# Optimization experiments

Hardware: AMD Instinct MI355X
Metric: run time of the kernel (lower is better)

## Reference

```python
import jax, jax.numpy as jnp
import numpy as np

B, T_IN, T_OUT, V, C = 2048, 10, 25, 22, 3
D = V * C            # embed / gru hidden = 66
H = 3                # attention heads
HD = D // H          # head dim = 22
EPS = 1e-5
DIMS = [(C, 64), (64, 32), (32, 64), (64, C)]


def _bn(x, g, b):
    # eval-mode BatchNorm2d with default running stats (mean=0, var=1)
    return x * (g / jnp.sqrt(1.0 + EPS))[None, :, None, None] + b[None, :, None, None]


def _gcn_layer(x, A, Tm, cw, cb, g, bt, rw, rb, rg, rbt, pre):
    # x: (N, Cin, T, V); STSGCN ST_GCNN_layer with 1x1 conv (kernel [1,1])
    res = _bn(jnp.einsum('nctv,oc->notv', x, rw) + rb[None, :, None, None], rg, rbt)
    y = jnp.einsum('nctv,vtq->ncqv', x, Tm)   # temporal mixing
    y = jnp.einsum('nctv,tvw->nctw', y, A)    # spatial (joint) mixing
    y = _bn(jnp.einsum('nctv,oc->notv', y, cw) + cb[None, :, None, None], g, bt)
    y = y + res
    return jnp.where(y >= 0, y, pre * y)      # PReLU (scalar slope)


def setup_inputs() -> dict:
    key = jax.random.key(0)
    ks = iter(jax.random.split(key, 64))
    def rn(shape, s=0.05):
        return jax.random.normal(next(ks), shape, dtype=jnp.float32) * s
    d = {"x": rn((B, T_IN, V, C), 1.0)}
    d["A"] = rn((4, T_IN, V, V), 0.2)
    d["Tm"] = rn((4, V, T_IN, T_IN), 0.3)
    d["pre"] = jnp.full((4,), 0.25, jnp.float32)
    for i, (ci, co) in enumerate(DIMS):
        d[f"cw{i}"] = rn((co, ci), 0.1)
        d[f"cb{i}"] = rn((co,), 0.1)
        d[f"g{i}"] = jnp.ones((co,), jnp.float32)
        d[f"bt{i}"] = jnp.zeros((co,), jnp.float32)
        d[f"rw{i}"] = rn((co, ci), 0.1)
        d[f"rb{i}"] = rn((co,), 0.1)
        d[f"rg{i}"] = jnp.ones((co,), jnp.float32)
        d[f"rbt{i}"] = jnp.zeros((co,), jnp.float32)
    d["gru_wi"] = rn((3 * D, D)); d["gru_wh"] = rn((3 * D, D))
    d["gru_bi"] = rn((3 * D,));   d["gru_bh"] = rn((3 * D,))
    d["qkv_w"] = rn((3 * D, D)); d["qkv_b"] = rn((3 * D,))
    d["ow"] = rn((D, D)); d["ob"] = rn((D,))
    d["lw"] = rn((D, 2 * D)); d["lb"] = rn((D,))
    return d


def _forward(x, A, Tm, pre, cws, cbs, gs, bts, rws, rbs, rgs, rbts,
             gru_wi, gru_wh, gru_bi, gru_bh, qkv_w, qkv_b, ow, ob, lw, lb):
    raw = x.reshape(B, T_IN, D)                 # (N,T,V*C), joint-major flatten
    h = jnp.transpose(x, (0, 3, 1, 2))          # (N,C,T,V)
    for i in range(4):
        h = _gcn_layer(h, A[i], Tm[i], cws[i], cbs[i], gs[i], bts[i],
                       rws[i], rbs[i], rgs[i], rbts[i], pre[i])
    enc = jnp.transpose(h, (0, 2, 3, 1)).reshape(B, T_IN, D)  # (N,T,V*C)

    wq, wk, wv = qkv_w[:D], qkv_w[D:2 * D], qkv_w[2 * D:]
    bq, bk, bv = qkv_b[:D], qkv_b[D:2 * D], qkv_b[2 * D:]
    # K,V of encoder sequence are constant across decode steps: project once
    k = (enc @ wk.T + bk).reshape(B, T_IN, H, HD)
    v = (enc @ wv.T + bv).reshape(B, T_IN, H, HD)
    scale = 1.0 / jnp.sqrt(jnp.float32(HD))

    def gru(inp, hprev):
        gi = inp @ gru_wi.T + gru_bi
        gh = hprev @ gru_wh.T + gru_bh
        ir, iz, inn = jnp.split(gi, 3, axis=-1)
        hr, hz, hn = jnp.split(gh, 3, axis=-1)
        r = jax.nn.sigmoid(ir + hr)
        z = jax.nn.sigmoid(iz + hz)
        n = jnp.tanh(inn + r * hn)
        return (1.0 - z) * n + z * hprev

    def step(carry, _):
        hs, tp = carry
        hs = gru(tp, hs)
        q = ((hs @ wq.T + bq) * scale).reshape(B, H, HD)
        scores = jnp.einsum('bhd,bthd->bht', q, k)
        attn = jax.nn.softmax(scores, axis=-1)
        ctx = jnp.einsum('bht,bthd->bhd', attn, v).reshape(B, D) @ ow.T + ob
        pred = jnp.concatenate([hs, ctx], axis=-1) @ lw.T + lb + tp  # residual
        return (hs, pred), pred

    h0 = enc[:, -1, :]
    tp0 = raw[:, -1, :]
    _, preds = jax.lax.scan(step, (h0, tp0), None, length=T_OUT)
    out = jnp.transpose(preds, (1, 0, 2))       # (N, T_out, D)
    return out.reshape(B, T_OUT, V, C)


def reference(x, A, Tm, pre,
              cw0, cb0, g0, bt0, rw0, rb0, rg0, rbt0,
              cw1, cb1, g1, bt1, rw1, rb1, rg1, rbt1,
              cw2, cb2, g2, bt2, rw2, rb2, rg2, rbt2,
              cw3, cb3, g3, bt3, rw3, rb3, rg3, rbt3,
              gru_wi, gru_wh, gru_bi, gru_bh, qkv_w, qkv_b, ow, ob, lw, lb):
    return _forward(x, A, Tm, pre,
                    [cw0, cw1, cw2, cw3], [cb0, cb1, cb2, cb3],
                    [g0, g1, g2, g3], [bt0, bt1, bt2, bt3],
                    [rw0, rw1, rw2, rw3], [rb0, rb1, rb2, rb3],
                    [rg0, rg1, rg2, rg3], [rbt0, rbt1, rbt2, rbt3],
                    gru_wi, gru_wh, gru_bi, gru_bh, qkv_w, qkv_b, ow, ob, lw, lb)
```

## Files before the change

kernel.cpp:

```cpp
#include <hip/hip_runtime.h>

#define DEV static __device__ __forceinline__


struct EncW {
  const float* cw[4]; const float* cb[4]; const float* g[4]; const float* bt[4];
  const float* rw[4]; const float* rb[4]; const float* rg[4]; const float* rbt[4];
};


template<int CI, int CO, int OGRAN>
DEV void gcn_orig(int tid,
    const float* __restrict__ cw, const float* __restrict__ cb,
    const float* __restrict__ gg, const float* __restrict__ bt,
    const float* __restrict__ rw, const float* __restrict__ rb,
    const float* __restrict__ rg, const float* __restrict__ rbt,
    const float* __restrict__ TmL, const float* __restrict__ AL, float preL,
    float* __restrict__ act, float* __restrict__ S,
    float* __restrict__ rmul, float* __restrict__ radd,
    float* __restrict__ cmul, float* __restrict__ cadd)
{
  constexpr int COP8 = (CO + 7) & ~7;
  constexpr int NT = (CO / OGRAN) * 55;
  constexpr int RWN = CI * COP8;
  static_assert(RWN + 2200 <= 4840, "rw+Tm co-stage must fit in S");
  const float inv = 0.99999499987f;

  for (int idx = tid; idx < RWN + 2200; idx += 512) {
    if (idx < RWN) {
      int c = idx / COP8, o = idx % COP8;
      S[idx] = (o < CO) ? rw[o * CI + c] : 0.f;
    } else {
      int j = idx - RWN;
      int tq = j / 22, v = j % 22;
      S[idx] = TmL[v * 100 + tq];
    }
  }
  for (int idx = tid; idx < 64; idx += 512) {
    bool ok = idx < CO;
    float rm = ok ? rg[idx] * inv : 0.f;
    float cm = ok ? gg[idx] * inv : 0.f;
    rmul[idx] = rm;
    radd[idx] = ok ? rb[idx] * rm + rbt[idx] : 0.f;
    cmul[idx] = cm;
    cadd[idx] = ok ? cb[idx] * cm + bt[idx] : 0.f;
  }
  __syncthreads();

  float racc[OGRAN * 4];
  const int og = tid / 55, pp = tid % 55;
  if (tid < NT) {
    #pragma unroll
    for (int k = 0; k < OGRAN * 4; ++k) racc[k] = 0.f;
    #pragma unroll 4
    for (int c = 0; c < CI; ++c) {
      const float* wr = S + c * COP8 + og * OGRAN;
      float4 av = *(const float4*)(act + c * 220 + pp * 4);
      float wv[OGRAN];
      if constexpr (OGRAN == 8) {
        float4 w0 = *(const float4*)(wr);
        float4 w1 = *(const float4*)(wr + 4);
        wv[0]=w0.x; wv[1]=w0.y; wv[2]=w0.z; wv[3]=w0.w;
        wv[4]=w1.x; wv[5]=w1.y; wv[6]=w1.z; wv[7]=w1.w;
      } else if constexpr (OGRAN == 4) {
        float4 w0 = *(const float4*)(wr);
        wv[0]=w0.x; wv[1]=w0.y; wv[2]=w0.z; wv[3]=w0.w;
      } else {
        wv[0] = wr[0];
      }
      #pragma unroll
      for (int o = 0; o < OGRAN; ++o) {
        racc[o*4+0] += wv[o]*av.x; racc[o*4+1] += wv[o]*av.y;
        racc[o*4+2] += wv[o]*av.z; racc[o*4+3] += wv[o]*av.w;
      }
    }
    #pragma unroll
    for (int o = 0; o < OGRAN; ++o) {
      float m = rmul[og * OGRAN + o], a = radd[og * OGRAN + o];
      #pragma unroll
      for (int k = 0; k < 4; ++k) racc[o*4+k] = racc[o*4+k]*m + a;
    }
  }
  __syncthreads();

  for (int idx = tid; idx < CI * 11; idx += 512) {
    int v2 = idx % 11, c = idx / 11;
    float* base = act + c * 220 + v2 * 2;
    float xin[10][2];
    #pragma unroll
    for (int t = 0; t < 10; ++t) { xin[t][0] = base[t*22]; xin[t][1] = base[t*22+1]; }
    float ya[10][2];
    #pragma unroll
    for (int q = 0; q < 10; ++q) { ya[q][0] = 0.f; ya[q][1] = 0.f; }
    #pragma unroll
    for (int t = 0; t < 10; ++t) {
      const float* tm = S + RWN + t * 220 + v2 * 2;
      #pragma unroll
      for (int q = 0; q < 10; ++q) {
        ya[q][0] += tm[q*22]   * xin[t][0];
        ya[q][1] += tm[q*22+1] * xin[t][1];
      }
    }
    #pragma unroll
    for (int q = 0; q < 10; ++q) { base[q*22] = ya[q][0]; base[q*22+1] = ya[q][1]; }
  }
  __syncthreads();

  for (int idx = tid; idx < 4840; idx += 512) S[idx] = AL[idx];
  __syncthreads();

  for (int idx = tid; idx < CI * 10; idx += 512) {
    int t = idx % 10, c = idx / 10;
    float* row = act + c * 220 + t * 22;
    float yin[22];
    #pragma unroll
    for (int v = 0; v < 22; ++v) yin[v] = row[v];
    float za[22];
    #pragma unroll
    for (int w = 0; w < 22; ++w) za[w] = 0.f;
    #pragma unroll 2
    for (int v = 0; v < 22; ++v) {
      const float* ar = S + (t * 22 + v) * 22;
      float y0 = yin[v];
      #pragma unroll
      for (int w = 0; w < 22; ++w) za[w] += y0 * ar[w];
    }
    #pragma unroll
    for (int w = 0; w < 22; ++w) row[w] = za[w];
  }
  __syncthreads();

  for (int idx = tid; idx < RWN; idx += 512) {
    int c = idx / COP8, o = idx % COP8;
    S[idx] = (o < CO) ? cw[o * CI + c] : 0.f;
  }
  __syncthreads();

  float cacc[OGRAN * 4];
  if (tid < NT) {
    #pragma unroll
    for (int k = 0; k < OGRAN * 4; ++k) cacc[k] = 0.f;
    #pragma unroll 4
    for (int c = 0; c < CI; ++c) {
      const float* wr = S + c * COP8 + og * OGRAN;
      float4 av = *(const float4*)(act + c * 220 + pp * 4);
      float wv[OGRAN];
      if constexpr (OGRAN == 8) {
        float4 w0 = *(const float4*)(wr);
        float4 w1 = *(const float4*)(wr + 4);
        wv[0]=w0.x; wv[1]=w0.y; wv[2]=w0.z; wv[3]=w0.w;
        wv[4]=w1.x; wv[5]=w1.y; wv[6]=w1.z; wv[7]=w1.w;
      } else if constexpr (OGRAN == 4) {
        float4 w0 = *(const float4*)(wr);
        wv[0]=w0.x; wv[1]=w0.y; wv[2]=w0.z; wv[3]=w0.w;
      } else {
        wv[0] = wr[0];
      }
      #pragma unroll
      for (int o = 0; o < OGRAN; ++o) {
        cacc[o*4+0] += wv[o]*av.x; cacc[o*4+1] += wv[o]*av.y;
        cacc[o*4+2] += wv[o]*av.z; cacc[o*4+3] += wv[o]*av.w;
      }
    }
  }
  __syncthreads();
  if (tid < NT) {
    #pragma unroll
    for (int o = 0; o < OGRAN; ++o) {
      float m = cmul[og * OGRAN + o], a = cadd[og * OGRAN + o];
      #pragma unroll
      for (int k = 0; k < 4; ++k) {
        float y = cacc[o*4+k]*m + a + racc[o*4+k];
        act[(og*OGRAN+o)*220 + pp*4 + k] = (y >= 0.f) ? y : preL * y;
      }
    }
  }
  __syncthreads();
}

template<int CI, int CO, int OGRAN>
DEV void gcn_reord(int tid,
    const float* __restrict__ cw, const float* __restrict__ cb,
    const float* __restrict__ gg, const float* __restrict__ bt,
    const float* __restrict__ rw, const float* __restrict__ rb,
    const float* __restrict__ rg, const float* __restrict__ rbt,
    const float* __restrict__ TmL, const float* __restrict__ AL, float preL,
    float* __restrict__ act, float* __restrict__ S,
    float* __restrict__ rmul, float* __restrict__ radd,
    float* __restrict__ cmul, float* __restrict__ cadd)
{
  constexpr int CO2 = 2 * CO;
  constexpr int COP8 = (CO2 + 7) & ~7;
  constexpr int NT = (CO2 / OGRAN) * 55;
  constexpr int RWN = CI * COP8;
  static_assert(RWN <= 4840, "W2 must fit in S");
  const float inv = 0.99999499987f;

  for (int idx = tid; idx < RWN; idx += 512) {
    int c = idx / COP8, o = idx % COP8;
    float w = 0.f;
    if (o < CO) w = cw[o * CI + c];
    else if (o < CO2) w = rw[(o - CO) * CI + c];
    S[idx] = w;
  }
  for (int idx = tid; idx < 64; idx += 512) {
    bool ok = idx < CO;
    float rm = ok ? rg[idx] * inv : 0.f;
    float cm = ok ? gg[idx] * inv : 0.f;
    rmul[idx] = rm;
    radd[idx] = ok ? rb[idx] * rm + rbt[idx] : 0.f;
    cmul[idx] = cm;
    cadd[idx] = ok ? cb[idx] * cm + bt[idx] : 0.f;
  }
  __syncthreads();

  float acc[OGRAN * 4];
  const int og = tid / 55, pp = tid % 55;
  if (tid < NT) {
    #pragma unroll
    for (int k = 0; k < OGRAN * 4; ++k) acc[k] = 0.f;
    #pragma unroll 4
    for (int c = 0; c < CI; ++c) {
      const float* wr = S + c * COP8 + og * OGRAN;
      float4 av = *(const float4*)(act + c * 220 + pp * 4);
      float wv[OGRAN];
      if constexpr (OGRAN == 8) {
        float4 w0 = *(const float4*)(wr);
        float4 w1 = *(const float4*)(wr + 4);
        wv[0]=w0.x; wv[1]=w0.y; wv[2]=w0.z; wv[3]=w0.w;
        wv[4]=w1.x; wv[5]=w1.y; wv[6]=w1.z; wv[7]=w1.w;
      } else if constexpr (OGRAN == 4) {
        float4 w0 = *(const float4*)(wr);
        wv[0]=w0.x; wv[1]=w0.y; wv[2]=w0.z; wv[3]=w0.w;
      } else {
        wv[0] = wr[0];
      }
      #pragma unroll
      for (int o = 0; o < OGRAN; ++o) {
        acc[o*4+0] += wv[o]*av.x; acc[o*4+1] += wv[o]*av.y;
        acc[o*4+2] += wv[o]*av.z; acc[o*4+3] += wv[o]*av.w;
      }
    }
  }
  __syncthreads();

  if (tid < NT) {
    #pragma unroll
    for (int o = 0; o < OGRAN; ++o) {
      const int oo = og * OGRAN + o;
      const bool isr = oo >= CO;
      const float m = isr ? rmul[oo - CO] : 1.f;
      const float a = isr ? radd[oo - CO] : 0.f;
      #pragma unroll
      for (int k = 0; k < 4; ++k)
        act[oo * 220 + pp * 4 + k] = acc[o*4+k] * m + a;
    }
  }
  for (int i = tid; i < 2200; i += 512) {
    int tq = i / 22, v = i % 22;
    S[i] = TmL[v * 100 + tq];
  }
  __syncthreads();

  for (int idx = tid; idx < CO * 11; idx += 512) {
    int v2 = idx % 11, c = idx / 11;
    float* base = act + c * 220 + v2 * 2;
    float xin[10][2];
    #pragma unroll
    for (int t = 0; t < 10; ++t) { xin[t][0] = base[t*22]; xin[t][1] = base[t*22+1]; }
    float ya[10][2];
    #pragma unroll
    for (int q = 0; q < 10; ++q) { ya[q][0] = 0.f; ya[q][1] = 0.f; }
    #pragma unroll
    for (int t = 0; t < 10; ++t) {
      const float* tm = S + t * 220 + v2 * 2;
      #pragma unroll
      for (int q = 0; q < 10; ++q) {
        ya[q][0] += tm[q*22]   * xin[t][0];
        ya[q][1] += tm[q*22+1] * xin[t][1];
      }
    }
    #pragma unroll
    for (int q = 0; q < 10; ++q) { base[q*22] = ya[q][0]; base[q*22+1] = ya[q][1]; }
  }
  __syncthreads();

  for (int idx = tid; idx < 4840; idx += 512) S[idx] = AL[idx];
  __syncthreads();

  for (int idx = tid; idx < CO * 10; idx += 512) {
    int t = idx % 10, c = idx / 10;
    float* row = act + c * 220 + t * 22;
    float yin[22];
    #pragma unroll
    for (int v = 0; v < 22; ++v) yin[v] = row[v];
    float za[22];
    #pragma unroll
    for (int w = 0; w < 22; ++w) za[w] = 0.f;
    #pragma unroll 2
    for (int v = 0; v < 22; ++v) {
      const float* ar = S + (t * 22 + v) * 22;
      float y0 = yin[v];
      #pragma unroll
      for (int w = 0; w < 22; ++w) za[w] += y0 * ar[w];
    }
    #pragma unroll
    for (int w = 0; w < 22; ++w) row[w] = za[w];
  }
  __syncthreads();

  for (int idx = tid; idx < CO * 220; idx += 512) {
    int o = idx / 220, p = idx % 220;
    float y = act[o * 220 + p] * cmul[o] + cadd[o] + act[(CO + o) * 220 + p];
    act[o * 220 + p] = (y >= 0.f) ? y : preL * y;
  }
  __syncthreads();
}

__global__ __launch_bounds__(512, 4)
void enc_kernel(const float* __restrict__ x, const float* __restrict__ A,
                const float* __restrict__ Tm, const float* __restrict__ pre, EncW W,
                const float* __restrict__ qkvT, const float* __restrict__ qkv_b,
                float* __restrict__ h0_ws, float* __restrict__ k_ws,
                float* __restrict__ v_ws)
{
  __shared__ __align__(16) float act[64 * 220];
  __shared__ __align__(16) float S[4840];
  __shared__ float rmul[64], radd[64], cmul[64], cadd[64];

  const int tid = threadIdx.x;
  const int b = blockIdx.x;

  for (int idx = tid; idx < 660; idx += 512) {
    int c = idx / 220, r = idx % 220, t = r / 22, v = r % 22;
    act[c * 220 + t * 22 + v] = x[(((size_t)b * 10 + t) * 22 + v) * 3 + c];
  }
  float p0 = pre[0], p1 = pre[1], p2 = pre[2], p3 = pre[3];

  gcn_orig<3, 64, 8>(tid, W.cw[0], W.cb[0], W.g[0], W.bt[0], W.rw[0], W.rb[0], W.rg[0], W.rbt[0],
                     Tm, A, p0, act, S, rmul, radd, cmul, cadd);
  gcn_reord<64, 32, 8>(tid, W.cw[1], W.cb[1], W.g[1], W.bt[1], W.rw[1], W.rb[1], W.rg[1], W.rbt[1],
                     Tm + 2200, A + 4840, p1, act, S, rmul, radd, cmul, cadd);
  gcn_orig<32, 64, 8>(tid, W.cw[2], W.cb[2], W.g[2], W.bt[2], W.rw[2], W.rb[2], W.rg[2], W.rbt[2],
                     Tm + 4400, A + 9680, p2, act, S, rmul, radd, cmul, cadd);
  gcn_reord<64, 3, 1>(tid, W.cw[3], W.cb[3], W.g[3], W.bt[3], W.rw[3], W.rb[3], W.rg[3], W.rbt[3],
                     Tm + 6600, A + 14520, p3, act, S, rmul, radd, cmul, cadd);

  float* encD = act + 3 * 220;
  for (int idx = tid; idx < 660; idx += 512) {
    int t = idx / 66, d = idx % 66, v = d / 3, c = d % 3;
    float val = act[c * 220 + t * 22 + v];
    encD[idx] = val;
    if (t == 9) h0_ws[(size_t)b * 66 + d] = val;
  }
  __syncthreads();

  for (int idx = tid; idx < 1320; idx += 512) {
    const int t = idx / 132, dd = idx % 132;
    const int row = 66 + dd;
    const float* wp = qkvT + row;
    const float* ep = encD + t * 66;
    float acc = 0.f;
    #pragma unroll 6
    for (int e = 0; e < 66; ++e) acc += wp[e * 198] * ep[e];
    acc += qkv_b[row];
    const int half = dd / 66, d = dd - half * 66;
    float* dst = half ? v_ws : k_ws;
    dst[(size_t)b * 660 + t * 66 + d] = acc;
  }
}


__global__ __launch_bounds__(512)
void prep_kernel(const float* __restrict__ qkv_w, const float* __restrict__ ow,
                 const float* __restrict__ ob, const float* __restrict__ lw,
                 const float* __restrict__ gru_wi, const float* __restrict__ gru_wh,
                 float* __restrict__ qkvT, float* __restrict__ wqD,
                 float* __restrict__ lwAT, float* __restrict__ MT,
                 float* __restrict__ cb2, float* __restrict__ wT_g)
{
  int idx = blockIdx.x * 512 + threadIdx.x;
  if (idx < 13068) {
    int e = idx / 198, j = idx % 198;
    qkvT[idx] = qkv_w[j * 66 + e];
    return;
  }
  int i1 = idx - 13068;
  if (i1 < 4356) {
    int e = i1 / 66, d = i1 % 66;
    wqD[i1] = qkv_w[d * 66 + e];
    return;
  }
  int i2 = i1 - 4356;
  if (i2 < 4356) {
    int e = i2 / 66, d = i2 % 66;
    lwAT[i2] = lw[d * 132 + e];
    return;
  }
  int i3 = i2 - 4356;
  if (i3 < 4356) {
    int e = i3 / 66, d = i3 % 66;
    const float* lrow = lw + d * 132 + 66;
    float acc = 0.f;
    for (int f = 0; f < 66; ++f) acc += lrow[f] * ow[f * 66 + e];
    MT[i3] = acc;
    return;
  }
  int i4 = i3 - 4356;
  if (i4 < 66) {
    const float* lrow = lw + i4 * 132 + 66;
    float acc = 0.f;
    for (int f = 0; f < 66; ++f) acc += lrow[f] * ob[f];
    cb2[i4] = acc;
    return;
  }
  int i5 = i4 - 66;
  if (i5 < 26136) {
    int e = i5 / 396, jm = i5 % 396;
    wT_g[i5] = (jm < 198) ? gru_wi[jm * 66 + e] : gru_wh[(jm - 198) * 66 + e];
  }
}


__global__ __launch_bounds__(512, 4)
void dec_kernel(const float* __restrict__ x, const float* __restrict__ h0_ws,
                const float* __restrict__ k_ws, const float* __restrict__ v_ws,
                const float* __restrict__ wT_g,
                const float* __restrict__ gru_bi, const float* __restrict__ gru_bh,
                const float* __restrict__ wqD, const float* __restrict__ qkv_b,
                const float* __restrict__ lwAT, const float* __restrict__ MT,
                const float* __restrict__ cb2, const float* __restrict__ lb,
                float* __restrict__ outp)
{
  __shared__ __align__(16) float kpS[7920];
  __shared__ __align__(16) float lwAS[4356];
  __shared__ __align__(16) float MS[4356];
  __shared__ __align__(16) float G[396 * 4];
  __shared__ __align__(16) float tpT[264], hsT[264], cxT[264];
  __shared__ float attnS[120];
  __shared__ float kbS[120];
  __shared__ float biS[198], bhS[198], lbS[66];

  const int tid = threadIdx.x;
  const int b0 = blockIdx.x * 4;
  const float qscale = 1.0f / sqrtf(22.0f);

  for (int idx = tid; idx < 4356; idx += 512) {
    lwAS[idx] = lwAT[idx]; MS[idx] = MT[idx];
  }
  for (int idx = tid; idx < 198; idx += 512) { biS[idx] = gru_bi[idx]; bhS[idx] = gru_bh[idx]; }
  for (int idx = tid; idx < 66; idx += 512)  { lbS[idx] = lb[idx] + cb2[idx]; }
  for (int idx = tid; idx < 264; idx += 512) {
    int d = idx >> 2, r = idx & 3;
    hsT[d * 4 + r] = h0_ws[(size_t)(b0 + r) * 66 + d];
    tpT[d * 4 + r] = x[(size_t)(b0 + r) * 660 + 594 + d];
  }
  for (int idx = tid; idx < 7920; idx += 512) {
    const int g = idx / 66, e = idx % 66;
    const int r = g / 30, rem = g % 30, h = rem / 10, t = rem % 10;
    const float* wq = wqD + e * 66 + h * 22;
    const float* kv = k_ws + (size_t)(b0 + r) * 660 + t * 66 + h * 22;
    float acc = 0.f;
    #pragma unroll
    for (int j = 0; j < 22; ++j) acc += wq[j] * kv[j];
    kpS[idx] = acc * qscale;
  }
  for (int idx = tid; idx < 120; idx += 512) {
    const int r = idx / 30, rem = idx % 30, h = rem / 10, t = rem % 10;
    const float* kv = k_ws + (size_t)(b0 + r) * 660 + t * 66 + h * 22;
    float acc = 0.f;
    #pragma unroll
    for (int j = 0; j < 22; ++j) acc += qkv_b[h * 22 + j] * kv[j];
    kbS[idx] = acc * qscale;
  }
  __syncthreads();

  for (int s = 0; s < 25; ++s) {
    if (tid < 198) {
      const bool lo = tid < 99;
      const int j0 = lo ? tid : (tid + 99);
      const int j1 = j0 + 99;
      const float* base = lo ? tpT : hsT;
      const float* w0 = wT_g + j0;
      const float* w1 = wT_g + j1;
      float a0 = 0.f, a1 = 0.f, a2 = 0.f, a3 = 0.f;
      float c0 = 0.f, c1 = 0.f, c2 = 0.f, c3 = 0.f;
      #pragma unroll 11
      for (int e = 0; e < 66; ++e) {
        float4 av = *(const float4*)(base + e * 4);
        const float wa = w0[e * 396];
        const float wb = w1[e * 396];
        a0 += wa * av.x; a1 += wa * av.y; a2 += wa * av.z; a3 += wa * av.w;
        c0 += wb * av.x; c1 += wb * av.y; c2 += wb * av.z; c3 += wb * av.w;
      }
      const float bias0 = lo ? biS[j0] : bhS[j0 - 198];
      const float bias1 = lo ? biS[j1] : bhS[j1 - 198];
      *(float4*)(G + j0 * 4) = make_float4(a0 + bias0, a1 + bias0, a2 + bias0, a3 + bias0);
      *(float4*)(G + j1 * 4) = make_float4(c0 + bias1, c1 + bias1, c2 + bias1, c3 + bias1);
    }
    __syncthreads();

    if (tid < 264) {
      int d = tid >> 2, r = tid & 3;
      float ir = G[d * 4 + r]         + G[(198 + d) * 4 + r];
      float iz = G[(66 + d) * 4 + r]  + G[(264 + d) * 4 + r];
      float nx = G[(132 + d) * 4 + r];
      float hn = G[(330 + d) * 4 + r];
      float rg = 1.f / (1.f + __expf(-ir));
      float zg = 1.f / (1.f + __expf(-iz));
      float t2 = __expf(2.f * (nx + rg * hn));
      float ng = 1.f - 2.f / (t2 + 1.f);
      float h = hsT[d * 4 + r];
      hsT[d * 4 + r] = (1.f - zg) * ng + zg * h;
    }
    __syncthreads();

    if (tid < 480) {
      const int g = tid >> 2, q4 = tid & 3;
      const int r = g / 30;
      const int e0 = q4 * 17;
      const int e1 = (q4 == 3) ? 66 : e0 + 17;
      const float* kpr = kpS + g * 66;
      float acc = 0.f;
      for (int e = e0; e < e1; ++e) acc += hsT[e * 4 + r] * kpr[e];
      acc += __shfl_xor(acc, 1);
      acc += __shfl_xor(acc, 2);
      if (q4 == 0) attnS[g] = acc + kbS[g];
    }
    __syncthreads();

    if (tid < 264) {
      int r = tid / 66, d = tid % 66, h = d / 22;
      const float* sp = attnS + (r * 3 + h) * 10;
      float sc[10];
      float mx = sp[0];
      #pragma unroll
      for (int t = 1; t < 10; ++t) { sc[t] = sp[t]; mx = fmaxf(mx, sp[t]); }
      sc[0] = sp[0];
      float sum = 0.f;
      #pragma unroll
      for (int t = 0; t < 10; ++t) { float e = __expf(sc[t] - mx); sc[t] = e; sum += e; }
      const float* vp = v_ws + (size_t)(b0 + r) * 660 + d;
      float acc = 0.f;
      #pragma unroll
      for (int t = 0; t < 10; ++t) acc += sc[t] * vp[t * 66];
      cxT[d * 4 + r] = acc / sum;
    }
    __syncthreads();

    if (tid < 264) {
      const int d = tid >> 2, q = tid & 3;
      const int e0 = q * 17;
      const int e1 = (q == 3) ? 66 : e0 + 17;
      float x0 = 0.f, x1 = 0.f, x2 = 0.f, x3 = 0.f;
      for (int e = e0; e < e1; ++e) {
        const float wa = lwAS[e * 66 + d];
        const float wm = MS[e * 66 + d];
        const float4 hv = *(const float4*)(hsT + e * 4);
        const float4 cv = *(const float4*)(cxT + e * 4);
        x0 += wa * hv.x + wm * cv.x;
        x1 += wa * hv.y + wm * cv.y;
        x2 += wa * hv.z + wm * cv.z;
        x3 += wa * hv.w + wm * cv.w;
      }
      x0 += __shfl_xor(x0, 1); x0 += __shfl_xor(x0, 2);
      x1 += __shfl_xor(x1, 1); x1 += __shfl_xor(x1, 2);
      x2 += __shfl_xor(x2, 1); x2 += __shfl_xor(x2, 2);
      x3 += __shfl_xor(x3, 1); x3 += __shfl_xor(x3, 2);
      const float val = (q == 0) ? x0 : (q == 1) ? x1 : (q == 2) ? x2 : x3;
      const float pred = val + lbS[d] + tpT[d * 4 + q];
      outp[((size_t)(b0 + q) * 25 + s) * 66 + d] = pred;
      tpT[d * 4 + q] = pred;
    }
    __syncthreads();
  }
}


extern "C" void kernel_launch(void* const* d_in, const int* in_sizes, int n_in,
                              void* d_out, int out_size, void* d_ws, size_t ws_size,
                              hipStream_t stream) {
  (void)in_sizes; (void)n_in; (void)out_size; (void)ws_size;
  const float* x   = (const float*)d_in[0];
  const float* A   = (const float*)d_in[1];
  const float* Tm  = (const float*)d_in[2];
  const float* pre = (const float*)d_in[3];
  EncW W;
  for (int i = 0; i < 4; ++i) {
    W.cw[i]  = (const float*)d_in[4 + 8 * i + 0];
    W.cb[i]  = (const float*)d_in[4 + 8 * i + 1];
    W.g[i]   = (const float*)d_in[4 + 8 * i + 2];
    W.bt[i]  = (const float*)d_in[4 + 8 * i + 3];
    W.rw[i]  = (const float*)d_in[4 + 8 * i + 4];
    W.rb[i]  = (const float*)d_in[4 + 8 * i + 5];
    W.rg[i]  = (const float*)d_in[4 + 8 * i + 6];
    W.rbt[i] = (const float*)d_in[4 + 8 * i + 7];
  }
  const float* gru_wi = (const float*)d_in[36];
  const float* gru_wh = (const float*)d_in[37];
  const float* gru_bi = (const float*)d_in[38];
  const float* gru_bh = (const float*)d_in[39];
  const float* qkv_w  = (const float*)d_in[40];
  const float* qkv_b  = (const float*)d_in[41];
  const float* ow     = (const float*)d_in[42];
  const float* ob     = (const float*)d_in[43];
  const float* lw     = (const float*)d_in[44];
  const float* lb     = (const float*)d_in[45];

  float* wsf  = (float*)d_ws;
  float* h0   = wsf;
  float* kw   = h0 + 2048 * 66;
  float* vw   = kw + 2048 * 660;
  float* qkvT = vw + 2048 * 660;
  float* wqD  = qkvT + 13068;
  float* lwAT = wqD + 4356;
  float* MT   = lwAT + 4356;
  float* cb2  = MT + 4356;
  float* wT_g = cb2 + 66;

  prep_kernel<<<103, 512, 0, stream>>>(qkv_w, ow, ob, lw, gru_wi, gru_wh,
                                       qkvT, wqD, lwAT, MT, cb2, wT_g);
  enc_kernel<<<2048, 512, 0, stream>>>(x, A, Tm, pre, W, qkvT, qkv_b, h0, kw, vw);
  dec_kernel<<<512, 512, 0, stream>>>(x, h0, kw, vw, wT_g, gru_bi, gru_bh,
                                      wqD, qkv_b, lwAT, MT, cb2, lb,
                                      (float*)d_out);
}
```

Measured before the change: 626.6 us.

## Stage A into free act rows to drop barriers; vectorize GRU weight loads

In the encoder GCN layers, the spatial mixing matrix A is staged into unused rows of the activation buffer instead of the shared scratch S. This lets the A load overlap with the temporal mixing and the conv weight staging, which removes one or two __syncthreads per layer. In the decoder, the GRU weight matrix is repacked in prep into groups of four input features, so each thread issues float4 global loads instead of strided scalar loads. Hidden-state buffers are padded with zeros to 68 elements to cover the extra lanes. The risk is that act rows used for A are not actually free, and the repacked weights add some padding work.

```diff
diff --git a/kernel.cpp b/kernel.cpp
--- a/kernel.cpp
+++ b/kernel.cpp
@@ -23,7 +23,9 @@
   constexpr int COP8 = (CO + 7) & ~7;
   constexpr int NT = (CO / OGRAN) * 55;
   constexpr int RWN = CI * COP8;
+  constexpr int AOFF = CI * 220;
   static_assert(RWN + 2200 <= 4840, "rw+Tm co-stage must fit in S");
+  static_assert(AOFF + 4840 <= 14080, "A must fit in free act rows");
   const float inv = 0.99999499987f;
 
   for (int idx = tid; idx < RWN + 2200; idx += 512) {
@@ -104,9 +106,11 @@
     #pragma unroll
     for (int q = 0; q < 10; ++q) { base[q*22] = ya[q][0]; base[q*22+1] = ya[q][1]; }
   }
-  __syncthreads();
-
-  for (int idx = tid; idx < 4840; idx += 512) S[idx] = AL[idx];
+  for (int i = tid; i < 4840; i += 512) act[AOFF + i] = AL[i];
+  for (int i = tid; i < RWN; i += 512) {
+    int c = i / COP8, o = i % COP8;
+    S[i] = (o < CO) ? cw[o * CI + c] : 0.f;
+  }
   __syncthreads();
 
   for (int idx = tid; idx < CI * 10; idx += 512) {
@@ -120,19 +124,13 @@
     for (int w = 0; w < 22; ++w) za[w] = 0.f;
     #pragma unroll 2
     for (int v = 0; v < 22; ++v) {
-      const float* ar = S + (t * 22 + v) * 22;
+      const float* ar = act + AOFF + (t * 22 + v) * 22;
       float y0 = yin[v];
       #pragma unroll
       for (int w = 0; w < 22; ++w) za[w] += y0 * ar[w];
     }
     #pragma unroll
     for (int w = 0; w < 22; ++w) row[w] = za[w];
-  }
-  __syncthreads();
-
-  for (int idx = tid; idx < RWN; idx += 512) {
-    int c = idx / COP8, o = idx % COP8;
-    S[idx] = (o < CO) ? cw[o * CI + c] : 0.f;
   }
   __syncthreads();
 
@@ -178,7 +176,7 @@
   __syncthreads();
 }
 
-template<int CI, int CO, int OGRAN>
+template<int CI, int CO, int OGRAN, int AOFF>
 DEV void gcn_reord(int tid,
     const float* __restrict__ cw, const float* __restrict__ cb,
     const float* __restrict__ gg, const float* __restrict__ bt,
@@ -194,6 +192,7 @@
   constexpr int NT = (CO2 / OGRAN) * 55;
   constexpr int RWN = CI * COP8;
   static_assert(RWN <= 4840, "W2 must fit in S");
+  static_assert(AOFF < 0 || AOFF + 4840 <= 14080, "A must fit in act");
   const float inv = 0.99999499987f;
 
   for (int idx = tid; idx < RWN; idx += 512) {
@@ -283,29 +282,37 @@
     #pragma unroll
     for (int q = 0; q < 10; ++q) { base[q*22] = ya[q][0]; base[q*22+1] = ya[q][1]; }
   }
-  __syncthreads();
-
-  for (int idx = tid; idx < 4840; idx += 512) S[idx] = AL[idx];
-  __syncthreads();
-
-  for (int idx = tid; idx < CO * 10; idx += 512) {
-    int t = idx % 10, c = idx / 10;
-    float* row = act + c * 220 + t * 22;
-    float yin[22];
-    #pragma unroll
-    for (int v = 0; v < 22; ++v) yin[v] = row[v];
-    float za[22];
-    #pragma unroll
-    for (int w = 0; w < 22; ++w) za[w] = 0.f;
-    #pragma unroll 2
-    for (int v = 0; v < 22; ++v) {
-      const float* ar = S + (t * 22 + v) * 22;
-      float y0 = yin[v];
-      #pragma unroll
-      for (int w = 0; w < 22; ++w) za[w] += y0 * ar[w];
-    }
-    #pragma unroll
-    for (int w = 0; w < 22; ++w) row[w] = za[w];
+  if constexpr (AOFF >= 0) {
+    for (int i = tid; i < 4840; i += 512) act[AOFF + i] = AL[i];
+  }
+  __syncthreads();
+
+  if constexpr (AOFF < 0) {
+    for (int idx = tid; idx < 4840; idx += 512) S[idx] = AL[idx];
+    __syncthreads();
+  }
+
+  {
+    const float* Abase = (AOFF >= 0) ? (act + AOFF) : S;
+    for (int idx = tid; idx < CO * 10; idx += 512) {
+      int t = idx % 10, c = idx / 10;
+      float* row = act + c * 220 + t * 22;
+      float yin[22];
+      #pragma unroll
+      for (int v = 0; v < 22; ++v) yin[v] = row[v];
+      float za[22];
+      #pragma unroll
+      for (int w = 0; w < 22; ++w) za[w] = 0.f;
+      #pragma unroll 2
+      for (int v = 0; v < 22; ++v) {
+        const float* ar = Abase + (t * 22 + v) * 22;
+        float y0 = yin[v];
+        #pragma unroll
+        for (int w = 0; w < 22; ++w) za[w] += y0 * ar[w];
+      }
+      #pragma unroll
+      for (int w = 0; w < 22; ++w) row[w] = za[w];
+    }
   }
   __syncthreads();
 
@@ -339,11 +346,11 @@
 
   gcn_orig<3, 64, 8>(tid, W.cw[0], W.cb[0], W.g[0], W.bt[0], W.rw[0], W.rb[0], W.rg[0], W.rbt[0],
                      Tm, A, p0, act, S, rmul, radd, cmul, cadd);
-  gcn_reord<64, 32, 8>(tid, W.cw[1], W.cb[1], W.g[1], W.bt[1], W.rw[1], W.rb[1], W.rg[1], W.rbt[1],
+  gcn_reord<64, 32, 8, -1>(tid, W.cw[1], W.cb[1], W.g[1], W.bt[1], W.rw[1], W.rb[1], W.rg[1], W.rbt[1],
                      Tm + 2200, A + 4840, p1, act, S, rmul, radd, cmul, cadd);
   gcn_orig<32, 64, 8>(tid, W.cw[2], W.cb[2], W.g[2], W.bt[2], W.rw[2], W.rb[2], W.rg[2], W.rbt[2],
                      Tm + 4400, A + 9680, p2, act, S, rmul, radd, cmul, cadd);
-  gcn_reord<64, 3, 1>(tid, W.cw[3], W.cb[3], W.g[3], W.bt[3], W.rw[3], W.rb[3], W.rg[3], W.rbt[3],
+  gcn_reord<64, 3, 1, 6 * 220>(tid, W.cw[3], W.cb[3], W.g[3], W.bt[3], W.rw[3], W.rb[3], W.rg[3], W.rbt[3],
                      Tm + 6600, A + 14520, p3, act, S, rmul, radd, cmul, cadd);
 
   float* encD = act + 3 * 220;
@@ -377,7 +384,7 @@
                  const float* __restrict__ gru_wi, const float* __restrict__ gru_wh,
                  float* __restrict__ qkvT, float* __restrict__ wqD,
                  float* __restrict__ lwAT, float* __restrict__ MT,
-                 float* __restrict__ cb2, float* __restrict__ wT_g)
+                 float* __restrict__ cb2, float* __restrict__ wT_g4)
 {
   int idx = blockIdx.x * 512 + threadIdx.x;
   if (idx < 13068) {
@@ -415,9 +422,14 @@
     return;
   }
   int i5 = i4 - 66;
-  if (i5 < 26136) {
-    int e = i5 / 396, jm = i5 % 396;
-    wT_g[i5] = (jm < 198) ? gru_wi[jm * 66 + e] : gru_wh[(jm - 198) * 66 + e];
+  if (i5 < 26928) {
+    int e4 = i5 / 1584, rem = i5 % 1584;
+    int jm = rem / 4, k = rem % 4;
+    int e = e4 * 4 + k;
+    float v = 0.f;
+    if (e < 66)
+      v = (jm < 198) ? gru_wi[jm * 66 + e] : gru_wh[(jm - 198) * 66 + e];
+    wT_g4[i5] = v;
   }
 }
 
@@ -425,7 +437,7 @@
 __global__ __launch_bounds__(512, 4)
 void dec_kernel(const float* __restrict__ x, const float* __restrict__ h0_ws,
                 const float* __restrict__ k_ws, const float* __restrict__ v_ws,
-                const float* __restrict__ wT_g,
+                const float* __restrict__ wT_g4,
                 const float* __restrict__ gru_bi, const float* __restrict__ gru_bh,
                 const float* __restrict__ wqD, const float* __restrict__ qkv_b,
                 const float* __restrict__ lwAT, const float* __restrict__ MT,
@@ -436,7 +448,7 @@
   __shared__ __align__(16) float lwAS[4356];
   __shared__ __align__(16) float MS[4356];
   __shared__ __align__(16) float G[396 * 4];
-  __shared__ __align__(16) float tpT[264], hsT[264], cxT[264];
+  __shared__ __align__(16) float tpT[272], hsT[272], cxT[264];
   __shared__ float attnS[120];
   __shared__ float kbS[120];
   __shared__ float biS[198], bhS[198], lbS[66];
@@ -455,6 +467,7 @@
     hsT[d * 4 + r] = h0_ws[(size_t)(b0 + r) * 66 + d];
     tpT[d * 4 + r] = x[(size_t)(b0 + r) * 660 + 594 + d];
   }
+  if (tid >= 264 && tid < 272) { hsT[tid] = 0.f; tpT[tid] = 0.f; }
   for (int idx = tid; idx < 7920; idx += 512) {
     const int g = idx / 66, e = idx % 66;
     const int r = g / 30, rem = g % 30, h = rem / 10, t = rem % 10;
@@ -481,17 +494,24 @@
       const int j0 = lo ? tid : (tid + 99);
       const int j1 = j0 + 99;
       const float* base = lo ? tpT : hsT;
-      const float* w0 = wT_g + j0;
-      const float* w1 = wT_g + j1;
       float a0 = 0.f, a1 = 0.f, a2 = 0.f, a3 = 0.f;
       float c0 = 0.f, c1 = 0.f, c2 = 0.f, c3 = 0.f;
-      #pragma unroll 11
-      for (int e = 0; e < 66; ++e) {
-        float4 av = *(const float4*)(base + e * 4);
-        const float wa = w0[e * 396];
-        const float wb = w1[e * 396];
-        a0 += wa * av.x; a1 += wa * av.y; a2 += wa * av.z; a3 += wa * av.w;
-        c0 += wb * av.x; c1 += wb * av.y; c2 += wb * av.z; c3 += wb * av.w;
+      #pragma unroll
+      for (int e4 = 0; e4 < 17; ++e4) {
+        const float4 wa = *(const float4*)(wT_g4 + (e4 * 396 + j0) * 4);
+        const float4 wb = *(const float4*)(wT_g4 + (e4 * 396 + j1) * 4);
+        const float4 av0 = *(const float4*)(base + (e4 * 4 + 0) * 4);
+        const float4 av1 = *(const float4*)(base + (e4 * 4 + 1) * 4);
+        const float4 av2 = *(const float4*)(base + (e4 * 4 + 2) * 4);
+        const float4 av3 = *(const float4*)(base + (e4 * 4 + 3) * 4);
+        a0 += wa.x*av0.x + wa.y*av1.x + wa.z*av2.x + wa.w*av3.x;
+        a1 += wa.x*av0.y + wa.y*av1.y + wa.z*av2.y + wa.w*av3.y;
+        a2 += wa.x*av0.z + wa.y*av1.z + wa.z*av2.z + wa.w*av3.z;
+        a3 += wa.x*av0.w + wa.y*av1.w + wa.z*av2.w + wa.w*av3.w;
+        c0 += wb.x*av0.x + wb.y*av1.x + wb.z*av2.x + wb.w*av3.x;
+        c1 += wb.x*av0.y + wb.y*av1.y + wb.z*av2.y + wb.w*av3.y;
+        c2 += wb.x*av0.z + wb.y*av1.z + wb.z*av2.z + wb.w*av3.z;
+        c3 += wb.x*av0.w + wb.y*av1.w + wb.z*av2.w + wb.w*av3.w;
       }
       const float bias0 = lo ? biS[j0] : bhS[j0 - 198];
       const float bias1 = lo ? biS[j1] : bhS[j1 - 198];
@@ -616,12 +636,12 @@
   float* lwAT = wqD + 4356;
   float* MT   = lwAT + 4356;
   float* cb2  = MT + 4356;
-  float* wT_g = cb2 + 66;
-
-  prep_kernel<<<103, 512, 0, stream>>>(qkv_w, ow, ob, lw, gru_wi, gru_wh,
-                                       qkvT, wqD, lwAT, MT, cb2, wT_g);
+  float* wTg4 = cb2 + 66;
+
+  prep_kernel<<<104, 512, 0, stream>>>(qkv_w, ow, ob, lw, gru_wi, gru_wh,
+                                       qkvT, wqD, lwAT, MT, cb2, wTg4);
   enc_kernel<<<2048, 512, 0, stream>>>(x, A, Tm, pre, W, qkvT, qkv_b, h0, kw, vw);
-  dec_kernel<<<512, 512, 0, stream>>>(x, h0, kw, vw, wT_g, gru_bi, gru_bh,
+  dec_kernel<<<512, 512, 0, stream>>>(x, h0, kw, vw, wTg4, gru_bi, gru_bh,
                                       wqD, qkv_b, lwAT, MT, cb2, lb,
                                       (float*)d_out);
 }
```

Result: slower. 1.998 ms (+218.9%).
